# Optimization experiments

Hardware: AMD Instinct MI355X
Metric: run time of the kernel (lower is better)

The kernel has to match this reference:

```python
import jax, jax.numpy as jnp
import numpy as np

STRIDES = (4, 8, 16, 32, 64)
FEAT = ((128, 128), (64, 64), (32, 32), (16, 16), (8, 8))
RATIOS = np.array([0.5, 1.0, 2.0], dtype=np.float64)
SCALE = 8.0
PRE_NMS = 2000
MAX_PER_IMG = 1000
NMS_THR = 0.7
MAX_SHAPE = (512, 512)
MAX_RATIO = float(abs(np.log(16.0 / 1000.0)))  # mmdet wh_ratio_clip default


def grid_anchors(H, W, stride):
    # mmdet AnchorGenerator: base_size = stride, center_offset = 0
    h_ratios = np.sqrt(RATIOS)
    w_ratios = 1.0 / h_ratios
    ws = stride * w_ratios * SCALE
    hs = stride * h_ratios * SCALE
    base = np.stack([-0.5 * ws, -0.5 * hs, 0.5 * ws, 0.5 * hs], axis=1)  # (A,4)
    sx = np.arange(W) * stride
    sy = np.arange(H) * stride
    yy, xx = np.meshgrid(sy, sx, indexing='ij')  # x varies fastest (mmdet order)
    shifts = np.stack([xx, yy, xx, yy], axis=-1).reshape(-1, 4)  # (H*W,4)
    return jnp.asarray((shifts[:, None, :] + base[None, :, :]).reshape(-1, 4), jnp.float32)


def level_candidates(cls, reg, anchors):
    # cls: (A,H,W), reg: (4A,H,W) -> location-major, anchor-minor flatten
    scores = jax.nn.sigmoid(jnp.transpose(cls, (1, 2, 0)).reshape(-1))
    deltas = jnp.transpose(reg, (1, 2, 0)).reshape(-1, 4)
    k = min(PRE_NMS, scores.shape[0])
    scores, idx = jax.lax.top_k(scores, k)
    return scores, deltas[idx], anchors[idx]


def decode(anchors, deltas):
    # DeltaXYWHBBoxCoder.decode with means=0, stds=1, max_shape=(512,512)
    px = (anchors[..., 0] + anchors[..., 2]) * 0.5
    py = (anchors[..., 1] + anchors[..., 3]) * 0.5
    pw = anchors[..., 2] - anchors[..., 0]
    ph = anchors[..., 3] - anchors[..., 1]
    dx, dy = deltas[..., 0], deltas[..., 1]
    dw = jnp.clip(deltas[..., 2], -MAX_RATIO, MAX_RATIO)
    dh = jnp.clip(deltas[..., 3], -MAX_RATIO, MAX_RATIO)
    gw = pw * jnp.exp(dw)
    gh = ph * jnp.exp(dh)
    gx = px + pw * dx
    gy = py + ph * dy
    x1 = jnp.clip(gx - gw * 0.5, 0.0, MAX_SHAPE[1])
    y1 = jnp.clip(gy - gh * 0.5, 0.0, MAX_SHAPE[0])
    x2 = jnp.clip(gx + gw * 0.5, 0.0, MAX_SHAPE[1])
    y2 = jnp.clip(gy + gh * 0.5, 0.0, MAX_SHAPE[0])
    return jnp.stack([x1, y1, x2, y2], axis=-1)


def nms_image(boxes, scores, levels):
    # boxes (M,4), scores (M,), levels (M,) int32. Fixed-shape greedy batched NMS;
    # invalid (zero-size, cf. filter_boxes with min_area=0) boxes get score -1 and are never kept.
    M = scores.shape[0]
    valid = ((boxes[:, 2] - boxes[:, 0]) > 0) & ((boxes[:, 3] - boxes[:, 1]) > 0)
    s = jnp.where(valid, scores, -1.0)
    order = jnp.argsort(-s)
    boxes_s = boxes[order]
    s = s[order]
    valid = valid[order]
    lev = levels[order]
    # batched_nms trick: offset each level so boxes of different levels never overlap
    off = lev.astype(boxes.dtype)[:, None] * (MAX_SHAPE[0] + 1.0)
    b = boxes_s + off
    x1, y1, x2, y2 = b[:, 0], b[:, 1], b[:, 2], b[:, 3]
    area = (x2 - x1) * (y2 - y1)
    iw = jnp.maximum(jnp.minimum(x2[:, None], x2[None, :]) - jnp.maximum(x1[:, None], x1[None, :]), 0.0)
    ih = jnp.maximum(jnp.minimum(y2[:, None], y2[None, :]) - jnp.maximum(y1[:, None], y1[None, :]), 0.0)
    inter = iw * ih
    union = area[:, None] + area[None, :] - inter
    iou = jnp.where(union > 0.0, inter / jnp.where(union > 0.0, union, 1.0), 0.0)  # (M,M)
    ar = jnp.arange(M)

    def body(i, keep):
        sup = keep[i] & (iou[i] > NMS_THR) & (ar > i)
        return keep & ~sup

    keep = jax.lax.fori_loop(0, M, body, valid)
    rank = jnp.cumsum(keep) - 1
    sel = keep & (rank < MAX_PER_IMG)
    dst = jnp.where(sel, rank, MAX_PER_IMG)  # overflow slot
    rows = jnp.concatenate([boxes_s, s[:, None]], axis=-1)
    rows = jnp.where(sel[:, None], rows, 0.0)
    out = jnp.zeros((MAX_PER_IMG + 1, 5), boxes.dtype).at[dst].set(rows)
    return out[:MAX_PER_IMG]


def setup_inputs() -> dict:
    key = jax.random.key(0)
    ks = jax.random.split(key, 10)
    d = {}
    for i, (h, w) in enumerate(FEAT):
        d[f'cls{i}'] = jax.random.normal(ks[i], (4, 3, h, w), dtype=jnp.float32)
        d[f'reg{i}'] = jax.random.normal(ks[5 + i], (4, 12, h, w), dtype=jnp.float32)
    return d


def reference(cls0, cls1, cls2, cls3, cls4, reg0, reg1, reg2, reg3, reg4):
    cls_list = [cls0, cls1, cls2, cls3, cls4]
    reg_list = [reg0, reg1, reg2, reg3, reg4]
    anchors = [grid_anchors(h, w, s) for (h, w), s in zip(FEAT, STRIDES)]
    sc, dl, an, lv = [], [], [], []
    for lvl in range(5):
        s, d, a = jax.vmap(level_candidates, in_axes=(0, 0, None))(cls_list[lvl], reg_list[lvl], anchors[lvl])
        sc.append(s); dl.append(d); an.append(a)
        lv.append(jnp.full(s.shape, lvl, jnp.int32))
    scores = jnp.concatenate(sc, axis=1)   # (N, M)
    deltas = jnp.concatenate(dl, axis=1)   # (N, M, 4)
    ancs = jnp.concatenate(an, axis=1)     # (N, M, 4)
    levels = jnp.concatenate(lv, axis=1)   # (N, M)
    boxes = decode(ancs, deltas)           # (N, M, 4)
    return jax.vmap(nms_image)(boxes, scores, levels)  # (N, 1000, 5)
```

## Files before the change

kernel.cpp:

```cpp
#include <hip/hip_runtime.h>
#include <cstdint>
#include <cstddef>

__constant__ int LV_N[5]    = {49152, 12288, 3072, 768, 192};
__constant__ int LV_K[5]    = {2000, 2000, 2000, 768, 192};
__constant__ int LV_OFF[5]  = {0, 2000, 4000, 6000, 6768};
__constant__ int LV_UOFF[5] = {0, 49152, 61440, 64512, 65280};
__constant__ int LV_W[5]    = {128, 64, 32, 16, 8};
__constant__ int LV_S[5]    = {4, 8, 16, 32, 64};
__constant__ int LV_LOGHW[5]= {14, 12, 10, 8, 6};
__constant__ int WPL[5]     = {32, 32, 32, 12, 3};
__constant__ int MOFF[5]    = {0, 70144, 140288, 210432, 221952};
__constant__ int MB_BASE[6] = {0, 256, 512, 768, 804, 807};
__constant__ int MB_CT[5]   = {8, 8, 8, 3, 1};
__constant__ int SGB6[6]    = {0, 12, 15, 16, 17, 18};

#define M_TOT 6960
#define U_PER_IMG 65472
#define MAX_OUT 1000
#define MWORDS_PER_IMG 223104
#define CAP 4096

struct Ptrs { const float* cls[5]; const float* reg[5]; };

#define MTH 0.7000000178813934326171875

__device__ __forceinline__ float xla_expf(float x) {
  const float exp_hi = 88.3762626647950f;
  const float exp_lo = -88.3762626647949f;
  const float log2ef = 1.44269504088896341f;
  const float c1 = 0.693359375f;
  const float c2 = -2.12194440e-4f;
  const float p0 = 1.9875691500e-4f;
  const float p1 = 1.3981999507e-3f;
  const float p2 = 8.3334519073e-3f;
  const float p3 = 4.1665795894e-2f;
  const float p4 = 1.6666665459e-1f;
  const float p5 = 5.0000001201e-1f;
  float xx = fminf(fmaxf(x, exp_lo), exp_hi);
  float fx = floorf(__fmaf_rn(xx, log2ef, 0.5f));
  float r = __fmaf_rn(fx, -c1, xx);
  r = __fmaf_rn(fx, -c2, r);
  float z = __fmul_rn(r, r);
  float y = __fmaf_rn(p0, r, p1);
  y = __fmaf_rn(y, r, p2);
  y = __fmaf_rn(y, r, p3);
  y = __fmaf_rn(y, r, p4);
  y = __fmaf_rn(y, r, p5);
  y = __fmaf_rn(y, z, r);
  y = __fadd_rn(y, 1.0f);
  int n = (int)fx;
  float two_n = __uint_as_float((unsigned)(n + 127) << 23);
  return __fmul_rn(y, two_n);
}

__device__ __forceinline__ float ref_sigmoid(float x) {
  return __fdiv_rn(1.0f, __fadd_rn(1.0f, xla_expf(-x)));
}

__global__ __launch_bounds__(256) void k_zero(uint4* ptr, int n4) {
  int i = (int)blockIdx.x * 256 + (int)threadIdx.x;
  if (i < n4) ptr[i] = make_uint4(0u, 0u, 0u, 0u);
}

__global__ __launch_bounds__(1024) void k_sig(Ptrs p, unsigned* u_arr,
                                              unsigned* ghist) {
  const int img = blockIdx.y;
  const int bx = blockIdx.x;
  int lvl = 0;
  while (bx >= SGB6[lvl + 1]) ++lvl;
  const int N = LV_N[lvl], LOGHW = LV_LOGHW[lvl];
  const int HW = 1 << LOGHW;
  const int e0 = (bx - SGB6[lvl]) * 4096;
  const int e1 = (e0 + 4096 < N) ? e0 + 4096 : N;
  const int tid = (int)threadIdx.x;
  __shared__ unsigned h[4096];
  for (int e = tid; e < 4096; e += 1024) h[e] = 0;
  __syncthreads();
  const float* cls = p.cls[lvl] + (size_t)img * N;
  unsigned* u = u_arr + img * U_PER_IMG + LV_UOFF[lvl];
  for (int e = e0 + tid; e < e1; e += 1024) {
    float logit = cls[e];
    unsigned ub = __float_as_uint(ref_sigmoid(logit));
    int a = e >> LOGHW, pix = e & (HW - 1);
    u[pix * 3 + a] = ub;
    atomicAdd(&h[(ub >> 18) & 4095u], 1u);
  }
  __syncthreads();
  unsigned* gh = ghist + (size_t)(img * 5 + lvl) * 4096;
  for (int e = tid; e < 4096; e += 1024)
    if (h[e]) atomicAdd(&gh[e], h[e]);
}

__global__ __launch_bounds__(1024) void k_thresh(const unsigned* u_arr,
    const unsigned* ghist, unsigned long long* T64_arr) {
  const int blk = blockIdx.x;
  const int img = blk / 5, lvl = blk % 5;
  const int N = LV_N[lvl], K = LV_K[lvl];
  const int tid = (int)threadIdx.x;
  if (N <= K) { if (tid == 0) T64_arr[blk] = 0ULL; return; }
  __shared__ unsigned h[4096], sA[4096], sB[4096];
  __shared__ unsigned sh_D, sh_sD, sh_sD1;
  const unsigned* u = u_arr + img * U_PER_IMG + LV_UOFF[lvl];

  for (int e = tid; e < 4096; e += 1024)
    h[e] = ghist[(size_t)blk * 4096 + e];
  __syncthreads();

  unsigned long long prefix = 0;
  unsigned want = (unsigned)K, above = 0;
  const int shifts[6] = {50, 38, 26, 14, 2, 0};
  const int widths[6] = {12, 12, 12, 12, 12, 2};
  for (int rd = 0; rd < 6; ++rd) {
    const int shift = shifts[rd], width = widths[rd];
    const int nb = 1 << width;
    if (rd > 0) {
      for (int e = tid; e < nb; e += 1024) h[e] = 0;
      __syncthreads();
      for (int i = tid; i < N; i += 1024) {
        unsigned long long key =
            ((unsigned long long)u[i] << 32) | (unsigned)(~(unsigned)i);
        if ((key >> (shift + width)) == prefix)
          atomicAdd(&h[(unsigned)(key >> shift) & (unsigned)(nb - 1)], 1u);
      }
      __syncthreads();
    }
    unsigned *Ap = sA, *Bp = sB;
    for (int e = tid; e < nb; e += 1024) Ap[e] = h[e];
    __syncthreads();
    for (int off = 1; off < nb; off <<= 1) {
      for (int e = tid; e < nb; e += 1024)
        Bp[e] = Ap[e] + ((e + off < nb) ? Ap[e + off] : 0u);
      __syncthreads();
      unsigned* t = Ap; Ap = Bp; Bp = t;
    }
    for (int e = tid; e < nb; e += 1024) {
      unsigned s = Ap[e], sn = (e + 1 < nb) ? Ap[e + 1] : 0u;
      if (s >= want && sn < want) { sh_D = (unsigned)e; sh_sD = s; sh_sD1 = sn; }
    }
    __syncthreads();
    unsigned D = sh_D, sD = sh_sD, sD1 = sh_sD1;
    unsigned long long npref = (prefix << width) | (unsigned long long)D;
    if (above + sD <= (unsigned)CAP || rd == 5) {
      if (tid == 0) T64_arr[blk] = npref << shift;
      return;
    }
    above += sD1; want -= sD1; prefix = npref;
    __syncthreads();
  }
}

__global__ __launch_bounds__(1024) void k_collect(const unsigned* u_arr,
    const unsigned long long* T64_arr, unsigned long long* gtk, unsigned* gcnt) {
  const int img = blockIdx.y;
  const int bx = blockIdx.x;
  int lvl = 0;
  while (bx >= SGB6[lvl + 1]) ++lvl;
  const int N = LV_N[lvl];
  const int e0 = (bx - SGB6[lvl]) * 4096;
  const int tid = (int)threadIdx.x;
  const int lane = tid & 63;
  const int w = tid >> 6;
  const unsigned long long T = T64_arr[img * 5 + lvl];
  const unsigned* u = u_arr + img * U_PER_IMG + LV_UOFF[lvl];

  __shared__ unsigned wcnt[64];

  unsigned long long key0 = 0, key1 = 0, key2 = 0, key3 = 0;
  unsigned long long bm0, bm1, bm2, bm3;
  {
    int e = e0 + 0 * 1024 + tid;
    bool pr = false;
    if (e < N) { key0 = ((unsigned long long)u[e] << 32) | (unsigned)(~(unsigned)e); pr = key0 >= T; }
    bm0 = __ballot(pr);
    if (lane == 0) wcnt[w * 4 + 0] = (unsigned)__popcll(bm0);
  }
  {
    int e = e0 + 1 * 1024 + tid;
    bool pr = false;
    if (e < N) { key1 = ((unsigned long long)u[e] << 32) | (unsigned)(~(unsigned)e); pr = key1 >= T; }
    bm1 = __ballot(pr);
    if (lane == 0) wcnt[w * 4 + 1] = (unsigned)__popcll(bm1);
  }
  {
    int e = e0 + 2 * 1024 + tid;
    bool pr = false;
    if (e < N) { key2 = ((unsigned long long)u[e] << 32) | (unsigned)(~(unsigned)e); pr = key2 >= T; }
    bm2 = __ballot(pr);
    if (lane == 0) wcnt[w * 4 + 2] = (unsigned)__popcll(bm2);
  }
  {
    int e = e0 + 3 * 1024 + tid;
    bool pr = false;
    if (e < N) { key3 = ((unsigned long long)u[e] << 32) | (unsigned)(~(unsigned)e); pr = key3 >= T; }
    bm3 = __ballot(pr);
    if (lane == 0) wcnt[w * 4 + 3] = (unsigned)__popcll(bm3);
  }
  __syncthreads();
  if (tid < 64) {
    unsigned c = wcnt[tid];
    unsigned pre = c;
    #pragma unroll
    for (int off = 1; off < 64; off <<= 1) {
      unsigned t = __shfl_up(pre, off);
      if (tid >= off) pre += t;
    }
    unsigned total = __shfl(pre, 63);
    unsigned base = 0;
    if (tid == 63 && total) base = atomicAdd(gcnt + (img * 5 + lvl), total);
    base = __shfl(base, 63);
    wcnt[tid] = base + pre - c;
  }
  __syncthreads();
  unsigned long long* dst = gtk + (size_t)(img * 5 + lvl) * CAP;
  const unsigned long long below = (1ULL << lane) - 1ULL;
  if ((bm0 >> lane) & 1ULL) {
    unsigned slot = wcnt[w * 4 + 0] + (unsigned)__popcll(bm0 & below);
    if (slot < (unsigned)CAP) dst[slot] = key0;
  }
  if ((bm1 >> lane) & 1ULL) {
    unsigned slot = wcnt[w * 4 + 1] + (unsigned)__popcll(bm1 & below);
    if (slot < (unsigned)CAP) dst[slot] = key1;
  }
  if ((bm2 >> lane) & 1ULL) {
    unsigned slot = wcnt[w * 4 + 2] + (unsigned)__popcll(bm2 & below);
    if (slot < (unsigned)CAP) dst[slot] = key2;
  }
  if ((bm3 >> lane) & 1ULL) {
    unsigned slot = wcnt[w * 4 + 3] + (unsigned)__popcll(bm3 & below);
    if (slot < (unsigned)CAP) dst[slot] = key3;
  }
}

__global__ __launch_bounds__(256) void k_rank(Ptrs p,
    const unsigned long long* gtk, const unsigned* gcnt,
    float* cand_box, float* cand_s, unsigned long long* vflags) {
  const int il = (int)blockIdx.y;
  const int img = il / 5, lvl = il % 5;
  const int N = LV_N[lvl], K = LV_K[lvl], W = LV_W[lvl], S = LV_S[lvl];
  const int HW = N / 3;
  const float* reg = p.reg[lvl] + (size_t)img * 12 * HW;
  const int tid = (int)threadIdx.x;
  unsigned cnt = gcnt[il];
  if (cnt > (unsigned)CAP) cnt = CAP;
  if ((unsigned)blockIdx.x * 256u >= cnt) return;
  const unsigned cnt32 = (cnt + 31u) & ~31u;
  __shared__ ulonglong2 keys2[CAP / 2];
  unsigned long long* keys = (unsigned long long*)keys2;
  const unsigned long long* src = gtk + (size_t)il * CAP;
  for (int e = tid; e < (int)cnt32; e += 256)
    keys[e] = (e < (int)cnt) ? src[e] : 0ULL;
  __syncthreads();
  const int s = (int)blockIdx.x * 256 + tid;
  if (s >= (int)cnt) return;
  const unsigned long long mykey = keys[s];
  unsigned r0 = 0, r1 = 0, r2 = 0, r3 = 0;
  const unsigned half = cnt32 >> 1;
  for (unsigned j = 0; j < half; j += 16) {
    #pragma unroll
    for (int q = 0; q < 16; q += 4) {
      ulonglong2 a = keys2[j + q + 0];
      ulonglong2 b = keys2[j + q + 1];
      ulonglong2 cc = keys2[j + q + 2];
      ulonglong2 d = keys2[j + q + 3];
      r0 += (a.x > mykey ? 1u : 0u) + (a.y > mykey ? 1u : 0u);
      r1 += (b.x > mykey ? 1u : 0u) + (b.y > mykey ? 1u : 0u);
      r2 += (cc.x > mykey ? 1u : 0u) + (cc.y > mykey ? 1u : 0u);
      r3 += (d.x > mykey ? 1u : 0u) + (d.y > mykey ? 1u : 0u);
    }
  }
  unsigned rank = r0 + r1 + r2 + r3;
  if (rank >= (unsigned)K) return;

  unsigned ubits = (unsigned)(mykey >> 32);
  unsigned idx = ~((unsigned)mykey);
  int a = (int)(idx % 3u); int pix = (int)(idx / 3u);
  int xq = pix % W, yq = pix / W;
  float dx = reg[(a * 4 + 0) * HW + pix];
  float dy = reg[(a * 4 + 1) * HW + pix];
  float dw = reg[(a * 4 + 2) * HW + pix];
  float dh = reg[(a * 4 + 3) * HW + pix];
  double rr = (a == 0) ? 0.5 : (a == 1 ? 1.0 : 2.0);
  double hr = sqrt(rr), wr = 1.0 / hr;
  double st = (double)S;
  double wsd = st * wr * 8.0, hsd = st * hr * 8.0;
  double sxd = (double)(xq * S), syd = (double)(yq * S);
  float a0 = (float)(sxd - 0.5 * wsd), a1 = (float)(syd - 0.5 * hsd);
  float a2 = (float)(sxd + 0.5 * wsd), a3 = (float)(syd + 0.5 * hsd);
  float px = __fmul_rn(__fadd_rn(a0, a2), 0.5f);
  float py = __fmul_rn(__fadd_rn(a1, a3), 0.5f);
  float pw = __fsub_rn(a2, a0), ph = __fsub_rn(a3, a1);
  const float MRf = 4.135166556742356f;
  float dwc = fminf(fmaxf(dw, -MRf), MRf);
  float dhc = fminf(fmaxf(dh, -MRf), MRf);
  float gw = __fmul_rn(pw, xla_expf(dwc));
  float gh = __fmul_rn(ph, xla_expf(dhc));
  float gx = __fmaf_rn(pw, dx, px);
  float gy = __fmaf_rn(ph, dy, py);
  float x1 = fminf(fmaxf(__fmaf_rn(gw, -0.5f, gx), 0.0f), 512.0f);
  float y1 = fminf(fmaxf(__fmaf_rn(gh, -0.5f, gy), 0.0f), 512.0f);
  float x2 = fminf(fmaxf(__fmaf_rn(gw,  0.5f, gx), 0.0f), 512.0f);
  float y2 = fminf(fmaxf(__fmaf_rn(gh,  0.5f, gy), 0.0f), 512.0f);
  bool valid = (__fsub_rn(x2, x1) > 0.0f) && (__fsub_rn(y2, y1) > 0.0f);
  int pos = img * M_TOT + LV_OFF[lvl] + (int)rank;
  cand_box[(size_t)pos * 4 + 0] = x1;
  cand_box[(size_t)pos * 4 + 1] = y1;
  cand_box[(size_t)pos * 4 + 2] = x2;
  cand_box[(size_t)pos * 4 + 3] = y2;
  float score = __uint_as_float(ubits);
  cand_s[pos] = valid ? score : -1.0f;
  if (valid)
    atomicOr(&vflags[(size_t)il * 32 + (rank >> 6)], 1ULL << (rank & 63));
}

__global__ __launch_bounds__(256) void k_part(const float* cand_box,
    const float* cand_s, const unsigned long long* vflags,
    float* n_x1, float* n_y1, float* n_x2, float* n_y2, float* n_ar,
    float* n_sc, unsigned* n_pos, unsigned* V_arr) {
  const int il = (int)blockIdx.x;
  const int img = il / 5, lvl = il % 5;
  const int K = LV_K[lvl];
  const int tid = (int)threadIdx.x;
  __shared__ unsigned long long sflag[32];
  __shared__ unsigned wpre[33];
  if (tid < 32) sflag[tid] = vflags[(size_t)il * 32 + tid];
  __syncthreads();
  if (tid < 32) {
    unsigned c = (unsigned)__popcll(sflag[tid]);
    #pragma unroll
    for (int off = 1; off < 32; off <<= 1) {
      unsigned t = __shfl_up(c, off);
      if (tid >= off) c += t;
    }
    wpre[tid + 1] = c;
    if (tid == 0) wpre[0] = 0;
  }
  __syncthreads();
  const unsigned V = wpre[32];
  const float offv = __fmul_rn((float)lvl, 513.0f);
  const int base = img * M_TOT + LV_OFF[lvl];
  for (int r = tid; r < K; r += 256) {
    unsigned long long word = sflag[r >> 6];
    unsigned fl = (unsigned)((word >> (r & 63)) & 1ULL);
    unsigned excl = wpre[r >> 6] +
                    (unsigned)__popcll(word & ((1ULL << (r & 63)) - 1ULL));
    unsigned pdst = fl ? excl : V + ((unsigned)r - excl);
    const float* b = cand_box + (size_t)(base + r) * 4;
    float ox1 = __fadd_rn(b[0], offv), oy1 = __fadd_rn(b[1], offv);
    float ox2 = __fadd_rn(b[2], offv), oy2 = __fadd_rn(b[3], offv);
    int dst = base + (int)pdst;
    n_x1[dst] = ox1; n_y1[dst] = oy1; n_x2[dst] = ox2; n_y2[dst] = oy2;
    n_ar[dst] = __fmul_rn(__fsub_rn(ox2, ox1), __fsub_rn(oy2, oy1));
    n_sc[dst] = cand_s[base + r];
    n_pos[dst] = (unsigned)(LV_OFF[lvl] + r);
  }
  if (tid == 0) V_arr[il] = V;
}

#define TSTAGE(S, M)                                                        \
  {                                                                         \
    unsigned long long t_ = __shfl_xor(x, S);                               \
    x = (lane & S) ? ((x & (M)) | ((t_ >> S) & ~(M)))                       \
                   : ((x & ~(M)) | ((t_ << S) & (M)));                      \
  }

__global__ __launch_bounds__(256) void k_mask(
    const float* n_x1, const float* n_y1, const float* n_x2, const float* n_y2,
    const float* n_ar, unsigned long long* mask, unsigned long long* diagT) {
  const int img = blockIdx.y;
  const int bx = blockIdx.x;
  int lvl = 0;
  while (bx >= MB_BASE[lvl + 1]) ++lvl;
  const int t = bx - MB_BASE[lvl];
  const int ct = MB_CT[lvl];
  const int rt = t / ct, c = t % ct;
  const int K = LV_K[lvl];
  const int row0 = rt * 64, col0 = c * 256;
  if (col0 + 255 <= row0) return;

  __shared__ float4 cb4[256];
  __shared__ float cba[256];
  __shared__ float4 rb4[64];
  __shared__ float rba[64];
  const int base = img * M_TOT + LV_OFF[lvl];
  const int tid = (int)threadIdx.x;
  if (tid < 64) {
    int r = row0 + tid;
    if (r < K) {
      rb4[tid] = make_float4(n_x1[base + r], n_y1[base + r],
                             n_x2[base + r], n_y2[base + r]);
      rba[tid] = n_ar[base + r];
    } else {
      rb4[tid] = make_float4(0.f, 0.f, 0.f, 0.f);
      rba[tid] = 0.f;
    }
  }
  {
    int j = col0 + tid;
    if (j < K) {
      cb4[tid] = make_float4(n_x1[base + j], n_y1[base + j],
                             n_x2[base + j], n_y2[base + j]);
      cba[tid] = n_ar[base + j];
    }
  }
  __syncthreads();
  const int wl = tid >> 6, lane = tid & 63;
  const int r = row0 + lane;
  const bool rvalid = (r < K);
  const float4 rb = rb4[lane];
  const float rar = rba[lane];
  unsigned long long word = 0ULL;
  const int jbase = wl * 64;
  const int jmax = K - col0 - jbase;
  #pragma unroll 16
  for (int k = 0; k < 64; ++k) {
    float4 cb = cb4[jbase + k];
    float car = cba[jbase + k];
    float iw = fmaxf(__fsub_rn(fminf(rb.z, cb.z), fmaxf(rb.x, cb.x)), 0.0f);
    float ih = fmaxf(__fsub_rn(fminf(rb.w, cb.w), fmaxf(rb.y, cb.y)), 0.0f);
    float inter = __fmul_rn(iw, ih);
    float uni = __fsub_rn(__fadd_rn(rar, car), inter);
    bool sup = (uni > 0.0f) && ((double)inter >= MTH * (double)uni);
    if (sup && k < jmax) word |= (1ULL << k);
  }
  if (!rvalid) word = 0ULL;
  if (rvalid)
    mask[(size_t)img * MWORDS_PER_IMG + MOFF[lvl] +
         (size_t)r * WPL[lvl] + (size_t)((col0 >> 6) + wl)] = word;
  if (col0 + (wl << 6) == row0) {
    unsigned long long x = word;
    TSTAGE(32, 0xFFFFFFFF00000000ULL)
    TSTAGE(16, 0xFFFF0000FFFF0000ULL)
    TSTAGE(8,  0xFF00FF00FF00FF00ULL)
    TSTAGE(4,  0xF0F0F0F0F0F0F0F0ULL)
    TSTAGE(2,  0xCCCCCCCCCCCCCCCCULL)
    TSTAGE(1,  0xAAAAAAAAAAAAAAAAULL)
    diagT[(size_t)(img * 5 + lvl) * (40 * 64) + (size_t)rt * 64 + lane] = x;
  }
}

#define SCAN_CHUNK(P0, P1, P2, P3)                                          \
  {                                                                         \
    const int r0 = c << 6;                                                  \
    if (w == (c & 7)) {                                                     \
      unsigned long long v = (g == (c >> 3)) ? aw : ~0ULL;                  \
      v &= __shfl_xor(v, 1);                                                \
      v &= __shfl_xor(v, 2);                                                \
      v &= __shfl_xor(v, 4);                                                \
      v &= __shfl_xor(v, 8);                                                \
      v = __shfl(v, (c >> 3) * 16);                                         \
      unsigned long long x = dg;                                            \
      unsigned long long kw = v;                                            \
      while (true) {                                                        \
        bool keep_j = (((v >> lane) & 1ULL) != 0ULL) &&                     \
                      ((kw & below & x) == 0ULL);                           \
        unsigned long long nkw = __ballot(keep_j);                          \
        if (nkw == kw) break;                                               \
        kw = nkw;                                                           \
      }                                                                     \
      if ((kw >> lane) & 1ULL)                                              \
        skept[kept + (int)__popcll(kw & below)] = (unsigned)(r0 + lane);    \
      if (lane == 0) s_kw[c & 1] = kw;                                      \
      int no_ = next_own < 40 ? next_own : 39;                              \
      dg = dT[(size_t)no_ * 64 + lane];                                     \
      next_own += 8;                                                        \
    }                                                                       \
    __syncthreads();                                                        \
    unsigned long long kwv = s_kw[c & 1];                                   \
    kept += (int)__popcll(kwv);                                             \
    aw &= ~(P0 & (unsigned long long)((long long)(kwv << (63 - (d0 + 0))) >> 63)); \
    aw &= ~(P1 & (unsigned long long)((long long)(kwv << (63 - (d0 + 1))) >> 63)); \
    aw &= ~(P2 & (unsigned long long)((long long)(kwv << (63 - (d0 + 2))) >> 63)); \
    aw &= ~(P3 & (unsigned long long)((long long)(kwv << (63 - (d0 + 3))) >> 63)); \
    P0 = mb[(size_t)(r0 + 128 + d0 + 0) * wpl + wkc];                       \
    P1 = mb[(size_t)(r0 + 128 + d0 + 1) * wpl + wkc];                       \
    P2 = mb[(size_t)(r0 + 128 + d0 + 2) * wpl + wkc];                       \
    P3 = mb[(size_t)(r0 + 128 + d0 + 3) * wpl + wkc];                       \
    ++c;                                                                    \
  }

__global__ __launch_bounds__(512) void k_scan(const unsigned long long* mask,
    const unsigned long long* diagT,
    const unsigned* n_pos, const float* n_sc, const unsigned* V_arr,
    unsigned* kept_pos, unsigned long long* kept_key, unsigned* kept_cnt) {
  const int il = (int)blockIdx.x;
  const int img = il / 5, lvl = il % 5;
  const int K = LV_K[lvl], wpl = WPL[lvl];
  const int tid = (int)threadIdx.x;
  const int w = tid >> 6, lane = tid & 63;
  const unsigned long long* mb =
      mask + (size_t)img * MWORDS_PER_IMG + MOFF[lvl];
  const unsigned long long* dT = diagT + (size_t)il * (40 * 64);

  __shared__ unsigned long long s_kw[2];
  __shared__ unsigned skept[MAX_OUT + 64];

  const int g = lane >> 4;
  const int wk = w + 8 * g;
  const int wkc = wk < wpl ? wk : 0;
  const int d0 = (lane & 15) * 4;
  const unsigned long long below = (1ULL << lane) - 1ULL;

  const int V = (int)V_arr[il];
  unsigned long long aw;
  {
    int lo = wk * 64, hi = V < lo + 64 ? V : lo + 64;
    aw = (hi > lo) ? ((hi - lo == 64) ? ~0ULL : ((1ULL << (hi - lo)) - 1ULL))
                   : 0ULL;
  }

  const int nchunks = (K + 63) >> 6;
  unsigned long long pfA0 = mb[(size_t)(d0 + 0) * wpl + wkc];
  unsigned long long pfA1 = mb[(size_t)(d0 + 1) * wpl + wkc];
  unsigned long long pfA2 = mb[(size_t)(d0 + 2) * wpl + wkc];
  unsigned long long pfA3 = mb[(size_t)(d0 + 3) * wpl + wkc];
  unsigned long long pfB0 = mb[(size_t)(64 + d0 + 0) * wpl + wkc];
  unsigned long long pfB1 = mb[(size_t)(64 + d0 + 1) * wpl + wkc];
  unsigned long long pfB2 = mb[(size_t)(64 + d0 + 2) * wpl + wkc];
  unsigned long long pfB3 = mb[(size_t)(64 + d0 + 3) * wpl + wkc];
  unsigned long long dg = dT[(size_t)w * 64 + lane];
  int next_own = w + 8;

  int kept = 0;
  int c = 0;
  while (c < nchunks && kept < MAX_OUT) {
    SCAN_CHUNK(pfA0, pfA1, pfA2, pfA3)
    if (c >= nchunks || kept >= MAX_OUT) break;
    SCAN_CHUNK(pfB0, pfB1, pfB2, pfB3)
  }

  __syncthreads();
  const int kc = kept < MAX_OUT ? kept : MAX_OUT;
  const int base = img * M_TOT + LV_OFF[lvl];
  const size_t bo = (size_t)il * 1024;
  for (int i = tid; i < kc; i += 512) {
    unsigned r = skept[i];
    unsigned pp = n_pos[base + (int)r];
    kept_pos[bo + i] = pp;
    kept_key[bo + i] =
        ((unsigned long long)__float_as_uint(n_sc[base + (int)r]) << 32) |
        (unsigned)(~pp);
  }
  if (tid == 0) kept_cnt[il] = (unsigned)kc;
}

__global__ __launch_bounds__(1024) void k_merge(const float* cand_box,
    const float* cand_s, const unsigned* kept_pos,
    const unsigned long long* kept_key, const unsigned* kept_cnt, float* out) {
  const int img = blockIdx.x;
  const int tid = (int)threadIdx.x;
  __shared__ unsigned cnts[5];
  __shared__ unsigned long long skey[5][1024];
  if (tid < 5) {
    unsigned c = kept_cnt[img * 5 + tid];
    cnts[tid] = c < (unsigned)MAX_OUT ? c : (unsigned)MAX_OUT;
  }
  __syncthreads();
  for (int e = tid; e < 5 * 1024; e += 1024) {
    int l = e >> 10, s = e & 1023;
    skey[l][s] = (s < (int)cnts[l])
        ? kept_key[(size_t)(img * 5 + l) * 1024 + s] : 0ULL;
  }
  __syncthreads();
  unsigned T = cnts[0] + cnts[1] + cnts[2] + cnts[3] + cnts[4];
  unsigned Tc = T < (unsigned)MAX_OUT ? T : (unsigned)MAX_OUT;
  for (int r = (int)Tc + tid; r < MAX_OUT; r += 1024) {
    float* o = out + (size_t)img * (MAX_OUT * 5) + (size_t)r * 5;
    o[0] = 0.f; o[1] = 0.f; o[2] = 0.f; o[3] = 0.f; o[4] = 0.f;
  }
  for (int e = tid; e < 5 * 1024; e += 1024) {
    int l = e >> 10, s = e & 1023;
    if (s >= (int)cnts[l]) continue;
    unsigned long long k0 = skey[l][s];
    unsigned rank = (unsigned)s;
    #pragma unroll
    for (int l2 = 0; l2 < 5; ++l2) {
      if (l2 == l) continue;
      int lo = 0, hi = (int)cnts[l2];
      while (lo < hi) {
        int mid = (lo + hi) >> 1;
        if (skey[l2][mid] > k0) lo = mid + 1; else hi = mid;
      }
      rank += (unsigned)lo;
    }
    if (rank < (unsigned)MAX_OUT) {
      unsigned pos = kept_pos[(size_t)(img * 5 + l) * 1024 + s];
      const float* b = cand_box + (size_t)(img * M_TOT + pos) * 4;
      float* o = out + (size_t)img * (MAX_OUT * 5) + (size_t)rank * 5;
      o[0] = b[0]; o[1] = b[1]; o[2] = b[2]; o[3] = b[3];
      o[4] = cand_s[img * M_TOT + pos];
    }
  }
}

extern "C" void kernel_launch(void* const* d_in, const int* in_sizes, int n_in,
                              void* d_out, int out_size, void* d_ws, size_t ws_size,
                              hipStream_t stream) {
  Ptrs p;
  bool interleaved = (n_in == 10 && in_sizes[1] == 4 * 12 * 128 * 128);
  for (int l = 0; l < 5; ++l) {
    if (interleaved) {
      p.cls[l] = (const float*)d_in[2 * l];
      p.reg[l] = (const float*)d_in[2 * l + 1];
    } else {
      p.cls[l] = (const float*)d_in[l];
      p.reg[l] = (const float*)d_in[5 + l];
    }
  }
  uint8_t* w = (uint8_t*)d_ws;
  size_t o = 0;
  auto carve = [&](size_t bytes) {
    void* ptr = w + o;
    o += (bytes + 255) & ~(size_t)255;
    return ptr;
  };
  unsigned* gcnt = (unsigned*)carve((size_t)20 * 4);
  unsigned* ghist = (unsigned*)carve((size_t)20 * 4096 * 4);
  unsigned long long* vflags = (unsigned long long*)carve((size_t)20 * 32 * 8);
  size_t zero_bytes = 256 + (size_t)20 * 4096 * 4 + (size_t)20 * 32 * 8;
  unsigned long long* T64_arr = (unsigned long long*)carve((size_t)20 * 8);
  unsigned* u_arr = (unsigned*)carve((size_t)4 * U_PER_IMG * 4);
  float* cand_box = (float*)carve((size_t)4 * M_TOT * 4 * 4);
  float* cand_s = (float*)carve((size_t)4 * M_TOT * 4);
  float* n_x1 = (float*)carve((size_t)4 * M_TOT * 4);
  float* n_y1 = (float*)carve((size_t)4 * M_TOT * 4);
  float* n_x2 = (float*)carve((size_t)4 * M_TOT * 4);
  float* n_y2 = (float*)carve((size_t)4 * M_TOT * 4);
  float* n_ar = (float*)carve((size_t)4 * M_TOT * 4);
  float* n_sc = (float*)carve((size_t)4 * M_TOT * 4);
  unsigned* n_pos = (unsigned*)carve((size_t)4 * M_TOT * 4);
  unsigned* V_arr = (unsigned*)carve((size_t)20 * 4);
  unsigned* kept_pos = (unsigned*)carve((size_t)4 * 5 * 1024 * 4);
  unsigned long long* kept_key = (unsigned long long*)carve((size_t)4 * 5 * 1024 * 8);
  unsigned* kept_cnt = (unsigned*)carve((size_t)20 * 4);
  unsigned long long* diagT = (unsigned long long*)carve((size_t)20 * 40 * 64 * 8);
  unsigned long long* mask = (unsigned long long*)carve((size_t)4 * MWORDS_PER_IMG * 8);
  unsigned long long* gtk = mask;
  (void)ws_size; (void)out_size;

  int n4 = (int)(zero_bytes >> 4);
  k_zero<<<(n4 + 255) / 256, 256, 0, stream>>>((uint4*)gcnt, n4);
  k_sig<<<dim3(18, 4), 1024, 0, stream>>>(p, u_arr, ghist);
  k_thresh<<<20, 1024, 0, stream>>>(u_arr, ghist, T64_arr);
  k_collect<<<dim3(18, 4), 1024, 0, stream>>>(u_arr, T64_arr, gtk, gcnt);
  k_rank<<<dim3(16, 20), 256, 0, stream>>>(p, gtk, gcnt, cand_box, cand_s,
                                           vflags);
  k_part<<<20, 256, 0, stream>>>(cand_box, cand_s, vflags,
      n_x1, n_y1, n_x2, n_y2, n_ar, n_sc, n_pos, V_arr);
  k_mask<<<dim3(807, 4), 256, 0, stream>>>(n_x1, n_y1, n_x2, n_y2, n_ar,
                                           mask, diagT);
  k_scan<<<20, 512, 0, stream>>>(mask, diagT, n_pos, n_sc, V_arr,
                                 kept_pos, kept_key, kept_cnt);
  k_merge<<<4, 1024, 0, stream>>>(cand_box, cand_s, kept_pos, kept_key,
                                  kept_cnt, (float*)d_out);
}
```

Measured before the change: 135.5 us.

## Coalesce sigmoid stores, use warp-shuffle scan in threshold, split merge per level

```diff
diff --git a/kernel.cpp b/kernel.cpp
--- a/kernel.cpp
+++ b/kernel.cpp
@@ -69,8 +69,7 @@
   const int bx = blockIdx.x;
   int lvl = 0;
   while (bx >= SGB6[lvl + 1]) ++lvl;
-  const int N = LV_N[lvl], LOGHW = LV_LOGHW[lvl];
-  const int HW = 1 << LOGHW;
+  const int N = LV_N[lvl];
   const int e0 = (bx - SGB6[lvl]) * 4096;
   const int e1 = (e0 + 4096 < N) ? e0 + 4096 : N;
   const int tid = (int)threadIdx.x;
@@ -82,8 +81,7 @@
   for (int e = e0 + tid; e < e1; e += 1024) {
     float logit = cls[e];
     unsigned ub = __float_as_uint(ref_sigmoid(logit));
-    int a = e >> LOGHW, pix = e & (HW - 1);
-    u[pix * 3 + a] = ub;
+    u[e] = ub;
     atomicAdd(&h[(ub >> 18) & 4095u], 1u);
   }
   __syncthreads();
@@ -96,52 +94,92 @@
     const unsigned* ghist, unsigned long long* T64_arr) {
   const int blk = blockIdx.x;
   const int img = blk / 5, lvl = blk % 5;
-  const int N = LV_N[lvl], K = LV_K[lvl];
+  const int N = LV_N[lvl], K = LV_K[lvl], LOGHW = LV_LOGHW[lvl];
+  const int HW = 1 << LOGHW;
   const int tid = (int)threadIdx.x;
+  const int lane = tid & 63, w = tid >> 6;
   if (N <= K) { if (tid == 0) T64_arr[blk] = 0ULL; return; }
-  __shared__ unsigned h[4096], sA[4096], sB[4096];
+  __shared__ unsigned h[4096];
+  __shared__ unsigned wsum[16], wsuf[16];
   __shared__ unsigned sh_D, sh_sD, sh_sD1;
   const unsigned* u = u_arr + img * U_PER_IMG + LV_UOFF[lvl];
-
-  for (int e = tid; e < 4096; e += 1024)
-    h[e] = ghist[(size_t)blk * 4096 + e];
-  __syncthreads();
 
   unsigned long long prefix = 0;
   unsigned want = (unsigned)K, above = 0;
   const int shifts[6] = {50, 38, 26, 14, 2, 0};
-  const int widths[6] = {12, 12, 12, 12, 12, 2};
   for (int rd = 0; rd < 6; ++rd) {
-    const int shift = shifts[rd], width = widths[rd];
-    const int nb = 1 << width;
-    if (rd > 0) {
-      for (int e = tid; e < nb; e += 1024) h[e] = 0;
+    const int shift = shifts[rd];
+    if (rd == 5) {
+      for (int e = tid; e < 4; e += 1024) h[e] = 0;
       __syncthreads();
-      for (int i = tid; i < N; i += 1024) {
+      for (int q = tid; q < N; q += 1024) {
+        unsigned a = (unsigned)q >> LOGHW, pix = (unsigned)q & (unsigned)(HW - 1);
+        unsigned ecl = pix * 3u + a;
         unsigned long long key =
-            ((unsigned long long)u[i] << 32) | (unsigned)(~(unsigned)i);
-        if ((key >> (shift + width)) == prefix)
-          atomicAdd(&h[(unsigned)(key >> shift) & (unsigned)(nb - 1)], 1u);
+            ((unsigned long long)u[q] << 32) | (unsigned)(~ecl);
+        if ((key >> 2) == prefix) atomicAdd(&h[(unsigned)key & 3u], 1u);
       }
       __syncthreads();
-    }
-    unsigned *Ap = sA, *Bp = sB;
-    for (int e = tid; e < nb; e += 1024) Ap[e] = h[e];
+      if (tid == 0) {
+        unsigned cum = 0; int D = 0;
+        for (int v = 3; v >= 0; --v) {
+          if (cum + h[v] >= want) { D = v; break; }
+          cum += h[v];
+        }
+        T64_arr[blk] = (prefix << 2) | (unsigned)D;
+      }
+      return;
+    }
+    if (rd == 0) {
+      for (int e = tid; e < 4096; e += 1024)
+        h[e] = ghist[(size_t)blk * 4096 + e];
+    } else {
+      for (int e = tid; e < 4096; e += 1024) h[e] = 0;
+      __syncthreads();
+      for (int q = tid; q < N; q += 1024) {
+        unsigned a = (unsigned)q >> LOGHW, pix = (unsigned)q & (unsigned)(HW - 1);
+        unsigned ecl = pix * 3u + a;
+        unsigned long long key =
+            ((unsigned long long)u[q] << 32) | (unsigned)(~ecl);
+        if ((key >> (shift + 12)) == prefix)
+          atomicAdd(&h[(unsigned)(key >> shift) & 4095u], 1u);
+      }
+    }
     __syncthreads();
-    for (int off = 1; off < nb; off <<= 1) {
-      for (int e = tid; e < nb; e += 1024)
-        Bp[e] = Ap[e] + ((e + off < nb) ? Ap[e + off] : 0u);
-      __syncthreads();
-      unsigned* t = Ap; Ap = Bp; Bp = t;
-    }
-    for (int e = tid; e < nb; e += 1024) {
-      unsigned s = Ap[e], sn = (e + 1 < nb) ? Ap[e + 1] : 0u;
-      if (s >= want && sn < want) { sh_D = (unsigned)e; sh_sD = s; sh_sD1 = sn; }
-    }
+    unsigned h0 = h[4 * tid + 0], h1 = h[4 * tid + 1];
+    unsigned h2 = h[4 * tid + 2], h3 = h[4 * tid + 3];
+    unsigned s = h0 + h1 + h2 + h3;
+    unsigned suf = s;
+    #pragma unroll
+    for (int off = 1; off < 64; off <<= 1) {
+      unsigned t2 = __shfl_down(suf, off);
+      if (lane + off < 64) suf += t2;
+    }
+    if (lane == 0) wsum[w] = suf;
+    __syncthreads();
+    if (tid < 16) {
+      unsigned v = wsum[tid];
+      #pragma unroll
+      for (int off = 1; off < 16; off <<= 1) {
+        unsigned t2 = __shfl_down(v, off);
+        if (tid + off < 16) v += t2;
+      }
+      wsuf[tid] = v;
+    }
+    __syncthreads();
+    unsigned Sth = ((w + 1 < 16) ? wsuf[w + 1] : 0u) + (suf - s);
+    unsigned f3 = Sth + h3;
+    unsigned f2 = f3 + h2;
+    unsigned f1 = f2 + h1;
+    unsigned f0 = f1 + h0;
+    if (f0 >= want && f1 < want) { sh_D = 4u * tid + 0; sh_sD = f0; sh_sD1 = f1; }
+    if (f1 >= want && f2 < want) { sh_D = 4u * tid + 1; sh_sD = f1; sh_sD1 = f2; }
+    if (f2 >= want && f3 < want) { sh_D = 4u * tid + 2; sh_sD = f2; sh_sD1 = f3; }
+    if (f3 >= want && Sth < want) { sh_D = 4u * tid + 3; sh_sD = f3; sh_sD1 = Sth; }
     __syncthreads();
     unsigned D = sh_D, sD = sh_sD, sD1 = sh_sD1;
-    unsigned long long npref = (prefix << width) | (unsigned long long)D;
-    if (above + sD <= (unsigned)CAP || rd == 5) {
+    unsigned long long npref = (prefix << 12) | (unsigned long long)D;
+    if (above + sD <= (unsigned)CAP) {
       if (tid == 0) T64_arr[blk] = npref << shift;
       return;
     }
@@ -156,7 +194,8 @@
   const int bx = blockIdx.x;
   int lvl = 0;
   while (bx >= SGB6[lvl + 1]) ++lvl;
-  const int N = LV_N[lvl];
+  const int N = LV_N[lvl], LOGHW = LV_LOGHW[lvl];
+  const int HW = 1 << LOGHW;
   const int e0 = (bx - SGB6[lvl]) * 4096;
   const int tid = (int)threadIdx.x;
   const int lane = tid & 63;
@@ -168,34 +207,42 @@
 
   unsigned long long key0 = 0, key1 = 0, key2 = 0, key3 = 0;
   unsigned long long bm0, bm1, bm2, bm3;
+  #define MKKEY(KV, Q)                                                      \
+    {                                                                       \
+      unsigned a_ = (unsigned)(Q) >> LOGHW;                                 \
+      unsigned pix_ = (unsigned)(Q) & (unsigned)(HW - 1);                   \
+      unsigned ecl_ = pix_ * 3u + a_;                                       \
+      KV = ((unsigned long long)u[Q] << 32) | (unsigned)(~ecl_);            \
+    }
   {
-    int e = e0 + 0 * 1024 + tid;
+    int q = e0 + 0 * 1024 + tid;
     bool pr = false;
-    if (e < N) { key0 = ((unsigned long long)u[e] << 32) | (unsigned)(~(unsigned)e); pr = key0 >= T; }
+    if (q < N) { MKKEY(key0, q) pr = key0 >= T; }
     bm0 = __ballot(pr);
     if (lane == 0) wcnt[w * 4 + 0] = (unsigned)__popcll(bm0);
   }
   {
-    int e = e0 + 1 * 1024 + tid;
+    int q = e0 + 1 * 1024 + tid;
     bool pr = false;
-    if (e < N) { key1 = ((unsigned long long)u[e] << 32) | (unsigned)(~(unsigned)e); pr = key1 >= T; }
+    if (q < N) { MKKEY(key1, q) pr = key1 >= T; }
     bm1 = __ballot(pr);
     if (lane == 0) wcnt[w * 4 + 1] = (unsigned)__popcll(bm1);
   }
   {
-    int e = e0 + 2 * 1024 + tid;
+    int q = e0 + 2 * 1024 + tid;
     bool pr = false;
-    if (e < N) { key2 = ((unsigned long long)u[e] << 32) | (unsigned)(~(unsigned)e); pr = key2 >= T; }
+    if (q < N) { MKKEY(key2, q) pr = key2 >= T; }
     bm2 = __ballot(pr);
     if (lane == 0) wcnt[w * 4 + 2] = (unsigned)__popcll(bm2);
   }
   {
-    int e = e0 + 3 * 1024 + tid;
+    int q = e0 + 3 * 1024 + tid;
     bool pr = false;
-    if (e < N) { key3 = ((unsigned long long)u[e] << 32) | (unsigned)(~(unsigned)e); pr = key3 >= T; }
+    if (q < N) { MKKEY(key3, q) pr = key3 >= T; }
     bm3 = __ballot(pr);
     if (lane == 0) wcnt[w * 4 + 3] = (unsigned)__popcll(bm3);
   }
+  #undef MKKEY
   __syncthreads();
   if (tid < 64) {
     unsigned c = wcnt[tid];
@@ -547,7 +594,8 @@
 __global__ __launch_bounds__(1024) void k_merge(const float* cand_box,
     const float* cand_s, const unsigned* kept_pos,
     const unsigned long long* kept_key, const unsigned* kept_cnt, float* out) {
-  const int img = blockIdx.x;
+  const int il = (int)blockIdx.x;
+  const int img = il / 5, l = il % 5;
   const int tid = (int)threadIdx.x;
   __shared__ unsigned cnts[5];
   __shared__ unsigned long long skey[5][1024];
@@ -557,39 +605,39 @@
   }
   __syncthreads();
   for (int e = tid; e < 5 * 1024; e += 1024) {
-    int l = e >> 10, s = e & 1023;
-    skey[l][s] = (s < (int)cnts[l])
-        ? kept_key[(size_t)(img * 5 + l) * 1024 + s] : 0ULL;
-  }
-  __syncthreads();
-  unsigned T = cnts[0] + cnts[1] + cnts[2] + cnts[3] + cnts[4];
-  unsigned Tc = T < (unsigned)MAX_OUT ? T : (unsigned)MAX_OUT;
-  for (int r = (int)Tc + tid; r < MAX_OUT; r += 1024) {
-    float* o = out + (size_t)img * (MAX_OUT * 5) + (size_t)r * 5;
-    o[0] = 0.f; o[1] = 0.f; o[2] = 0.f; o[3] = 0.f; o[4] = 0.f;
-  }
-  for (int e = tid; e < 5 * 1024; e += 1024) {
-    int l = e >> 10, s = e & 1023;
-    if (s >= (int)cnts[l]) continue;
-    unsigned long long k0 = skey[l][s];
-    unsigned rank = (unsigned)s;
-    #pragma unroll
-    for (int l2 = 0; l2 < 5; ++l2) {
-      if (l2 == l) continue;
-      int lo = 0, hi = (int)cnts[l2];
-      while (lo < hi) {
-        int mid = (lo + hi) >> 1;
-        if (skey[l2][mid] > k0) lo = mid + 1; else hi = mid;
-      }
-      rank += (unsigned)lo;
-    }
-    if (rank < (unsigned)MAX_OUT) {
-      unsigned pos = kept_pos[(size_t)(img * 5 + l) * 1024 + s];
-      const float* b = cand_box + (size_t)(img * M_TOT + pos) * 4;
-      float* o = out + (size_t)img * (MAX_OUT * 5) + (size_t)rank * 5;
-      o[0] = b[0]; o[1] = b[1]; o[2] = b[2]; o[3] = b[3];
-      o[4] = cand_s[img * M_TOT + pos];
-    }
+    int l2 = e >> 10, s = e & 1023;
+    skey[l2][s] = (s < (int)cnts[l2])
+        ? kept_key[(size_t)(img * 5 + l2) * 1024 + s] : 0ULL;
+  }
+  __syncthreads();
+  if (l == 0) {
+    unsigned T = cnts[0] + cnts[1] + cnts[2] + cnts[3] + cnts[4];
+    unsigned Tc = T < (unsigned)MAX_OUT ? T : (unsigned)MAX_OUT;
+    for (int r = (int)Tc + tid; r < MAX_OUT; r += 1024) {
+      float* o = out + (size_t)img * (MAX_OUT * 5) + (size_t)r * 5;
+      o[0] = 0.f; o[1] = 0.f; o[2] = 0.f; o[3] = 0.f; o[4] = 0.f;
+    }
+  }
+  const int s = tid;
+  if (s >= (int)cnts[l]) return;
+  unsigned long long k0 = skey[l][s];
+  unsigned rank = (unsigned)s;
+  #pragma unroll
+  for (int l2 = 0; l2 < 5; ++l2) {
+    if (l2 == l) continue;
+    int lo = 0, hi = (int)cnts[l2];
+    while (lo < hi) {
+      int mid = (lo + hi) >> 1;
+      if (skey[l2][mid] > k0) lo = mid + 1; else hi = mid;
+    }
+    rank += (unsigned)lo;
+  }
+  if (rank < (unsigned)MAX_OUT) {
+    unsigned pos = kept_pos[(size_t)(img * 5 + l) * 1024 + s];
+    const float* b = cand_box + (size_t)(img * M_TOT + pos) * 4;
+    float* o = out + (size_t)img * (MAX_OUT * 5) + (size_t)rank * 5;
+    o[0] = b[0]; o[1] = b[1]; o[2] = b[2]; o[3] = b[3];
+    o[4] = cand_s[img * M_TOT + pos];
   }
 }
 
@@ -651,6 +699,6 @@
                                            mask, diagT);
   k_scan<<<20, 512, 0, stream>>>(mask, diagT, n_pos, n_sc, V_arr,
                                  kept_pos, kept_key, kept_cnt);
-  k_merge<<<4, 1024, 0, stream>>>(cand_box, cand_s, kept_pos, kept_key,
-                                  kept_cnt, (float*)d_out);
-}
+  k_merge<<<20, 1024, 0, stream>>>(cand_box, cand_s, kept_pos, kept_key,
+                                   kept_cnt, (float*)d_out);
+}
```

After: 116.5 us. 1.16x faster.
